# Performance work log

Hardware: AMD Instinct MI355X
Metric: run time of the kernel (lower is better)

The kernel has to match this reference:

```python
import jax, jax.numpy as jnp
import numpy as np
from jax.scipy.special import erf

N_POINTS = 4096
N_EVENTS = 1000000
BETA = 1.0   # init_beta, constant (not a Parameter in the torch module)
ALPHA = 1.0  # torch.ones((1,1)) buffer
WEIGHT = 1.0


def setup_inputs() -> dict:
    key = jax.random.key(0)
    k1, k2, k3, k4, k5 = jax.random.split(key, 5)
    return {
        "z0": jax.random.uniform(k1, (N_POINTS, 2), dtype=jnp.float32),
        "v0": jax.random.uniform(k2, (N_POINTS, 2), dtype=jnp.float32),
        "event_times": jax.random.uniform(k3, (N_EVENTS,), dtype=jnp.float32),
        "t0": jnp.zeros((), dtype=jnp.float32),
        "tn": jnp.ones((), dtype=jnp.float32),
        "u_idx": jax.random.randint(k4, (N_EVENTS,), 0, N_POINTS, dtype=jnp.int64) if jax.config.read('jax_enable_x64') else jax.random.randint(k4, (N_EVENTS,), 0, N_POINTS).astype(jnp.int32),
        "v_idx": jax.random.randint(k5, (N_EVENTS,), 0, N_POINTS).astype(jnp.int32),
    }


def reference(z0, v0, event_times, t0, tn, u_idx, v_idx):
    beta = jnp.float32(BETA)
    alpha = jnp.float32(ALPHA)

    # ---- event term: sum_e beta - ||z_u(t_e) - z_v(t_e)||^2,  z(t) = z0 + v0*t (a0 == 0)
    dz0 = z0[u_idx] - z0[v_idx]                      # [E, 2]
    dv0 = v0[u_idx] - v0[v_idx]                      # [E, 2]
    dz = dz0 + dv0 * event_times[:, None]            # [E, 2]
    d2 = jnp.sum(dz * dz, axis=-1)                   # [E]
    event_intensity = jnp.sum(beta - d2)

    # ---- non-event term: analytic Hawkes integral over all triu pairs
    i, j = jnp.triu_indices(z0.shape[0], k=1)        # static, [P]
    a = z0[i, 0] - z0[j, 0]
    b = z0[i, 1] - z0[j, 1]
    m = v0[i, 0] - v0[j, 0]
    n = v0[i, 1] - v0[j, 1]
    mn2 = m * m + n * n                              # [P]
    s = jnp.sqrt(alpha * mn2)
    cross = a * n - b * m
    dot = a * m + b * n
    expo = jnp.exp((-(cross * cross) * alpha + mn2 * beta) / mn2)
    sqrt_pi = jnp.float32(np.sqrt(np.pi))
    integral = (-sqrt_pi * expo
                * (erf(alpha * (mn2 * t0 + dot) / s) - erf(alpha * (mn2 * tn + dot) / s))
                / (2.0 * s))                          # [P]
    non_event_intensity = jnp.sum(integral)

    return event_intensity - WEIGHT * non_event_intensity
```

## Files before the change

kernel.cpp:

```cpp
#include <hip/hip_runtime.h>

typedef float v2f __attribute__((ext_vector_type(2)));
typedef unsigned int v2u __attribute__((ext_vector_type(2)));

#define NPTS   4096
#define NEVT   1000000
#define NQUAD  (NEVT / 4)
#define TILE   64
#define NT     (NPTS / TILE)
#define PAIR_BLOCKS (NT * (NT + 1) / 2)
#define BLK    1024
#define GRID   512
#define NWAVES (GRID * (BLK / 64))
#define NUNIT2 (PAIR_BLOCKS * 32)
#define PERW2  (NUNIT2 / NWAVES)
#define REMW2  (NUNIT2 % NWAVES)

#define LOG2E  1.4426950408889634f
#define EA1 0.278393f
#define EA2 0.230389f
#define EA3 0.000972f
#define EA4 0.078108f

__device__ __forceinline__ v2f vabs2(v2f x) {
    return (v2f){__builtin_fabsf(x.x), __builtin_fabsf(x.y)};
}
__device__ __forceinline__ v2f signed_one_minus(v2f q, v2f s) {
    v2f r = (v2f){1.0f, 1.0f} - q;
    v2u ru, su;
    __builtin_memcpy(&ru, &r, 8);
    __builtin_memcpy(&su, &s, 8);
    ru |= (su & (v2u){0x80000000u, 0x80000000u});
    v2f o;
    __builtin_memcpy(&o, &ru, 8);
    return o;
}

__global__ __launch_bounds__(BLK, 4) void hawkes_fused(
    const float* __restrict__ z0, const float* __restrict__ v0,
    const float* __restrict__ et, const float* __restrict__ t0p,
    const float* __restrict__ tnp, const int* __restrict__ uix,
    const int* __restrict__ vix, float* __restrict__ out)
{
    __shared__ float sx[NPTS], sy[NPTS], sz[NPTS], sw[NPTS];
    __shared__ float red[BLK / 64];
    const int tid = threadIdx.x;

    const float t0 = *t0p;
    const float tn = *tnp;

    {
        const float4* z4 = (const float4*)z0;
        const float4* v4 = (const float4*)v0;
        #pragma unroll
        for (int k = 0; k < NPTS / (2 * BLK); ++k) {
            int p2 = tid + k * BLK;
            float4 zz = z4[p2];
            float4 vv = v4[p2];
            sx[2 * p2] = zz.x; sx[2 * p2 + 1] = zz.z;
            sy[2 * p2] = zz.y; sy[2 * p2 + 1] = zz.w;
            sz[2 * p2] = vv.x; sz[2 * p2 + 1] = vv.z;
            sw[2 * p2] = vv.y; sw[2 * p2 + 1] = vv.w;
        }
    }
    __syncthreads();

    float acc_ev = 0.0f;
    {
        int ev0 = (int)(((long long)blockIdx.x * NQUAD) / GRID);
        int ev1 = (int)(((long long)(blockIdx.x + 1) * NQUAD) / GRID);
        int q = ev0 + tid;
        if (q < ev1) {
            int base = q * 4;
            float4 t4 = *(const float4*)(et + base);
            int4   u4 = *(const int4*)(uix + base);
            int4   v4 = *(const int4*)(vix + base);
            float tt[4] = {t4.x, t4.y, t4.z, t4.w};
            int   uu[4] = {u4.x, u4.y, u4.z, u4.w};
            int   vv[4] = {v4.x, v4.y, v4.z, v4.w};
            #pragma unroll
            for (int e = 0; e < 4; ++e) {
                int a = uu[e], b = vv[e];
                float dx = __builtin_fmaf(sz[a] - sz[b], tt[e], sx[a] - sx[b]);
                float dy = __builtin_fmaf(sw[a] - sw[b], tt[e], sy[a] - sy[b]);
                acc_ev += 1.0f - (dx * dx + dy * dy);
            }
        }
    }

    const v2f t0v = (v2f){t0, t0};
    const v2f tnv = (v2f){tn, tn};
    const v2f l2e = (v2f){LOG2E, LOG2E};
    const int il  = tid & 63;
    const int wid = (int)blockIdx.x * (BLK / 64) + (tid >> 6);
    int u    = wid * PERW2 + (wid < REMW2 ? wid : REMW2);
    int uend = u + PERW2 + (wid < REMW2 ? 1 : 0);
    v2f accp = (v2f){0.0f, 0.0f};
    while (u < uend) {
        int L = u >> 5;
        int bi = (int)((129.0f - sqrtf((float)(16641 - 8 * L))) * 0.5f);
        while (bi * NT - bi * (bi - 1) / 2 > L) --bi;
        while ((bi + 1) * NT - (bi + 1) * bi / 2 <= L) ++bi;
        int bj = bi + (L - (bi * NT - bi * (bi - 1) / 2));
        int ibase = bi * TILE, jbase = bj * TILE;
        int i = ibase + il;
        v2f pix = (v2f){sx[i], sx[i]};
        v2f piy = (v2f){sy[i], sy[i]};
        v2f piz = (v2f){sz[i], sz[i]};
        v2f piw = (v2f){sw[i], sw[i]};
        int run_end = (L + 1) << 5;
        if (run_end > uend) run_end = uend;
        for (; u < run_end; ++u) {
            int j0 = jbase + ((u & 31) << 1);
            v2f tjx = *(const v2f*)&sx[j0];
            v2f tjy = *(const v2f*)&sy[j0];
            v2f tjz = *(const v2f*)&sz[j0];
            v2f tjw = *(const v2f*)&sw[j0];
            v2f a  = pix - tjx;
            v2f b  = piy - tjy;
            v2f m  = piz - tjz;
            v2f n  = piw - tjw;
            v2f mn2 = m * m + n * n;
            v2f cr  = a * n - b * m;
            v2f dt  = a * m + b * n;
            v2f invs = (v2f){__builtin_amdgcn_rsqf(mn2.x),
                             __builtin_amdgcn_rsqf(mn2.y)};
            v2f g   = cr * cr * (invs * invs);
            v2f exv = l2e - g * l2e;
            v2f ee  = (v2f){__builtin_amdgcn_exp2f(exv.x),
                            __builtin_amdgcn_exp2f(exv.y)};
            v2f A   = (mn2 * t0v + dt) * invs;
            v2f B   = (mn2 * tnv + dt) * invs;
            v2f xA  = vabs2(A), xB = vabs2(B);
            v2f PA  = (v2f){1.0f,1.0f} + xA*((v2f){EA1,EA1} + xA*((v2f){EA2,EA2}
                        + xA*((v2f){EA3,EA3} + xA*(v2f){EA4,EA4})));
            v2f PB  = (v2f){1.0f,1.0f} + xB*((v2f){EA1,EA1} + xB*((v2f){EA2,EA2}
                        + xB*((v2f){EA3,EA3} + xB*(v2f){EA4,EA4})));
            v2f PP  = PA * PB;
            v2f R   = (v2f){__builtin_amdgcn_rcpf(PP.x),
                            __builtin_amdgcn_rcpf(PP.y)};
            v2f rA  = R * PB, rB = R * PA;
            v2f qA  = rA * rA; qA *= qA;
            v2f qB  = rB * rB; qB *= qB;
            v2f eA  = signed_one_minus(qA, A);
            v2f eB  = signed_one_minus(qB, B);
            v2f term = (eB - eA) * ee * invs;
            v2f sel = (v2f){ (j0     > i) ? term.x : 0.0f,
                             (j0 + 1 > i) ? term.y : 0.0f };
            accp += sel;
        }
    }

    float contrib = __builtin_fmaf(-0.8862269254527580f, accp.x + accp.y, acc_ev);

    #pragma unroll
    for (int off = 32; off > 0; off >>= 1)
        contrib += __shfl_down(contrib, off, 64);
    if ((tid & 63) == 0) red[tid >> 6] = contrib;
    __syncthreads();
    if (tid == 0) {
        float s = 0.0f;
        #pragma unroll
        for (int w = 0; w < BLK / 64; ++w) s += red[w];
        atomicAdd(out, s);
    }
}

extern "C" void kernel_launch(void* const* d_in, const int* in_sizes, int n_in,
                              void* d_out, int out_size, void* d_ws, size_t ws_size,
                              hipStream_t stream) {
    const float* z0  = (const float*)d_in[0];
    const float* v0  = (const float*)d_in[1];
    const float* et  = (const float*)d_in[2];
    const float* t0p = (const float*)d_in[3];
    const float* tnp = (const float*)d_in[4];
    const int*   uix = (const int*)d_in[5];
    const int*   vix = (const int*)d_in[6];
    float* out = (float*)d_out;

    hipLaunchKernelGGL(hawkes_fused, dim3(GRID), dim3(BLK), 0, stream,
                       z0, v0, et, t0p, tnp, uix, vix, out);
}
```

Baseline: 87.26 us.

## Halve block size and assign fixed half-tile pair units to waves

Cuts the block size from 1024 to 512 threads. The pair integral is no longer split into evenly balanced per-wave ranges of column-pair steps. Instead each wave takes fixed half-tile units of 16 fully unrolled iterations, chosen by a grid-stride loop. Events are now mapped one quad per thread. The aim is to drop loop bookkeeping and run-boundary logic, but with 4160 units over 4096 waves a few waves do twice the work, which adds a tail.

```diff
diff --git a/kernel.cpp b/kernel.cpp
--- a/kernel.cpp
+++ b/kernel.cpp
@@ -9,12 +9,10 @@
 #define TILE   64
 #define NT     (NPTS / TILE)
 #define PAIR_BLOCKS (NT * (NT + 1) / 2)
-#define BLK    1024
+#define BLK    512
 #define GRID   512
 #define NWAVES (GRID * (BLK / 64))
-#define NUNIT2 (PAIR_BLOCKS * 32)
-#define PERW2  (NUNIT2 / NWAVES)
-#define REMW2  (NUNIT2 % NWAVES)
+#define NUNITS (PAIR_BLOCKS * 2)
 
 #define LOG2E  1.4426950408889634f
 #define EA1 0.278393f
@@ -51,12 +49,12 @@
 
     {
         const float4* z4 = (const float4*)z0;
-        const float4* v4 = (const float4*)v0;
+        const float4* vv4 = (const float4*)v0;
         #pragma unroll
         for (int k = 0; k < NPTS / (2 * BLK); ++k) {
             int p2 = tid + k * BLK;
             float4 zz = z4[p2];
-            float4 vv = v4[p2];
+            float4 vv = vv4[p2];
             sx[2 * p2] = zz.x; sx[2 * p2 + 1] = zz.z;
             sy[2 * p2] = zz.y; sy[2 * p2 + 1] = zz.w;
             sz[2 * p2] = vv.x; sz[2 * p2 + 1] = vv.z;
@@ -67,10 +65,8 @@
 
     float acc_ev = 0.0f;
     {
-        int ev0 = (int)(((long long)blockIdx.x * NQUAD) / GRID);
-        int ev1 = (int)(((long long)(blockIdx.x + 1) * NQUAD) / GRID);
-        int q = ev0 + tid;
-        if (q < ev1) {
+        int q = (int)blockIdx.x * BLK + tid;
+        if (q < NQUAD) {
             int base = q * 4;
             float4 t4 = *(const float4*)(et + base);
             int4   u4 = *(const int4*)(uix + base);
@@ -93,25 +89,24 @@
     const v2f l2e = (v2f){LOG2E, LOG2E};
     const int il  = tid & 63;
     const int wid = (int)blockIdx.x * (BLK / 64) + (tid >> 6);
-    int u    = wid * PERW2 + (wid < REMW2 ? wid : REMW2);
-    int uend = u + PERW2 + (wid < REMW2 ? 1 : 0);
     v2f accp = (v2f){0.0f, 0.0f};
-    while (u < uend) {
-        int L = u >> 5;
+    for (int un = wid; un < NUNITS; un += NWAVES) {
+        int L    = un >> 1;
+        int half = un & 1;
         int bi = (int)((129.0f - sqrtf((float)(16641 - 8 * L))) * 0.5f);
         while (bi * NT - bi * (bi - 1) / 2 > L) --bi;
         while ((bi + 1) * NT - (bi + 1) * bi / 2 <= L) ++bi;
         int bj = bi + (L - (bi * NT - bi * (bi - 1) / 2));
-        int ibase = bi * TILE, jbase = bj * TILE;
+        int ibase = bi * TILE;
+        int jb    = bj * TILE + (half << 5);
         int i = ibase + il;
         v2f pix = (v2f){sx[i], sx[i]};
         v2f piy = (v2f){sy[i], sy[i]};
         v2f piz = (v2f){sz[i], sz[i]};
         v2f piw = (v2f){sw[i], sw[i]};
-        int run_end = (L + 1) << 5;
-        if (run_end > uend) run_end = uend;
-        for (; u < run_end; ++u) {
-            int j0 = jbase + ((u & 31) << 1);
+        #pragma unroll
+        for (int k = 0; k < 16; ++k) {
+            int j0 = jb + (k << 1);
             v2f tjx = *(const v2f*)&sx[j0];
             v2f tjy = *(const v2f*)&sy[j0];
             v2f tjz = *(const v2f*)&sz[j0];
```

New measurement: 83.12 us. -4.7%, faster.
